# Performance work log

Hardware: AMD Instinct MI355X
Metric: run time of the kernel (lower is better)

## Reference

```python
import jax, jax.numpy as jnp
import numpy as np

N_NODES = 20000
DEG = 6
E = N_NODES * DEG  # 120000 edges == line-graph nodes
D_NODE, D_EDGE = 64, 16
HID, OUT = 128, 128
EPS = 1e-5


def setup_inputs() -> dict:
    key = jax.random.key(0)
    ks = jax.random.split(key, 8)
    rng = np.random.default_rng(0)
    # graph: each node is the source of DEG edges (direction='out' -> index_r = edge_index[0])
    src = np.repeat(np.arange(N_NODES), DEG)
    dst = rng.integers(0, N_NODES, E)
    edge_index = np.stack([src, dst]).astype(np.int64)
    # two_step_index: ordered pairs of distinct edges sharing a source node
    # (bipartite 2-hop, self loops removed), then GATConv add_self_loops re-appends (i,i)
    ii, jj = np.meshgrid(np.arange(DEG), np.arange(DEG), indexing='ij')
    off = ~np.eye(DEG, dtype=bool)
    ii, jj = ii[off], jj[off]  # DEG*(DEG-1) within-group pairs
    base = (np.arange(N_NODES) * DEG)[:, None]
    s2 = np.concatenate([(base + ii[None, :]).ravel(), np.arange(E)])
    d2 = np.concatenate([(base + jj[None, :]).ravel(), np.arange(E)])
    index_2step = np.stack([s2, d2]).astype(np.int64)  # [2, 720000]
    d_in = D_NODE + D_EDGE
    return {
        "edge_attr": jax.random.normal(ks[0], (E, D_EDGE), jnp.float32),
        "node_attr": jax.random.normal(ks[1], (N_NODES, D_NODE), jnp.float32),
        "bn0_g": jnp.ones((d_in,), jnp.float32),
        "bn0_b": jnp.zeros((d_in,), jnp.float32),
        "W1": jax.random.normal(ks[2], (d_in, HID), jnp.float32) / np.sqrt(d_in).astype(np.float32),
        "bn1_g": jnp.ones((HID,), jnp.float32),
        "bn1_b": jnp.zeros((HID,), jnp.float32),
        "Wg": jax.random.normal(ks[3], (HID, OUT), jnp.float32) / np.sqrt(HID).astype(np.float32),
        "att_src": jax.random.normal(ks[4], (OUT,), jnp.float32) * 0.1,
        "att_dst": jax.random.normal(ks[5], (OUT,), jnp.float32) * 0.1,
        "gat_bias": jnp.zeros((OUT,), jnp.float32),
        "bnf_g": jnp.ones((OUT,), jnp.float32),
        "bnf_b": jnp.zeros((OUT,), jnp.float32),
        "edge_index": jnp.asarray(edge_index),
        "index_2step": jnp.asarray(index_2step),
        "num_nodes": N_NODES,
    }


def batch_norm(x, g, b):
    # training-mode BatchNorm1d (biased variance), like the torch module default
    mu = x.mean(0)
    var = x.var(0)
    return (x - mu) * jax.lax.rsqrt(var + EPS) * g + b


def reference(edge_attr, node_attr, bn0_g, bn0_b, W1, bn1_g, bn1_b,
              Wg, att_src, att_dst, gat_bias, bnf_g, bnf_b,
              edge_index, index_2step, num_nodes):
    index_r = edge_index[0]  # [E] source node of each edge (direction='out')
    # h0: per-edge concat of source-node attrs and edge attrs  [E, Dn+De]
    h0 = jnp.concatenate([node_attr[index_r], edge_attr], axis=1)
    # linear encoder: BN -> Linear(no bias) -> BN -> ReLU (dropout p=0)
    h1 = jax.nn.relu(batch_norm(batch_norm(h0, bn0_g, bn0_b) @ W1, bn1_g, bn1_b))
    # --- GATConv (heads=1) on the line graph given by index_2step ---
    E_ = h1.shape[0]
    x = h1 @ Wg                 # [E, OUT]
    a_src = x @ att_src         # [E]
    a_dst = x @ att_dst         # [E]
    s, d = index_2step[0], index_2step[1]
    e = jax.nn.leaky_relu(a_src[s] + a_dst[d], 0.2)          # [E2]
    e = e - jax.ops.segment_max(e, d, num_segments=E_)[d]    # stable edge-softmax
    ex = jnp.exp(e)
    alpha = ex / (jax.ops.segment_sum(ex, d, num_segments=E_)[d] + 1e-16)
    h2 = jax.ops.segment_sum(alpha[:, None] * x[s], d, num_segments=E_) + gat_bias
    # --- global_add_pool keyed by source node id, then final BatchNorm ---
    h3 = jax.ops.segment_sum(h2, index_r, num_segments=num_nodes)  # [N, OUT]
    return batch_norm(h3, bnf_g, bnf_b)
```

## Files before the change

kernel.cpp:

```cpp
#include <hip/hip_runtime.h>

#define N_NODES 20000
#define DEG 6
#define E_EDGES 120000
#define EPS_BN 1e-5f

#define WS_S0SUM 0
#define WS_S0SQ  80
#define WS_S1SUM 160
#define WS_S1SQ  1184
#define WS_FSUM  2208
#define WS_FSQ   3232
#define WS_STATS_FLOATS 4256

#define LDA0 104
#define LDH1 136

typedef float f32x4 __attribute__((ext_vector_type(4)));
typedef short bf16x8 __attribute__((ext_vector_type(8)));

__device__ __forceinline__ unsigned short f2bf(float f) {
  unsigned u = __float_as_uint(f);
  u += 0x7fffu + ((u >> 16) & 1u);
  return (unsigned short)(u >> 16);
}
__device__ __forceinline__ unsigned pack2bf(float a, float b) {
  return (unsigned)f2bf(a) | ((unsigned)f2bf(b) << 16);
}
__device__ __forceinline__ bf16x8 load_w_frag(const float* __restrict__ W,
                                              int col, int k0, int kmax) {
  union { bf16x8 v; unsigned u[4]; } tmp;
  #pragma unroll
  for (int p = 0; p < 4; ++p) {
    int k = k0 + 2 * p;
    float a = (k < kmax) ? W[k * 128 + col] : 0.f;
    float b = (k + 1 < kmax) ? W[(k + 1) * 128 + col] : 0.f;
    tmp.u[p] = pack2bf(a, b);
  }
  return tmp.v;
}

__global__ __launch_bounds__(256) void k1_bn0_stats(
    const float* __restrict__ node_attr, const float* __restrict__ edge_attr,
    float* __restrict__ ws) {
  __shared__ float red[256];
  const int t = threadIdx.x;
  const int b = blockIdx.x;
  if (b < 128) {
    const int c = t & 63, rl = t >> 6;
    float s = 0.f, q = 0.f;
    for (int row = b * 4 + rl; row < N_NODES; row += 512) {
      float v = node_attr[row * 64 + c];
      s += v; q += v * v;
    }
    red[t] = s;
    __syncthreads();
    if (t < 64) atomicAdd(&ws[WS_S0SUM + t], red[t] + red[t + 64] + red[t + 128] + red[t + 192]);
    __syncthreads();
    red[t] = q;
    __syncthreads();
    if (t < 64) atomicAdd(&ws[WS_S0SQ + t], red[t] + red[t + 64] + red[t + 128] + red[t + 192]);
  } else {
    const int c = t & 15, rl = t >> 4;
    float s = 0.f, q = 0.f;
    for (int row = (b - 128) * 16 + rl; row < E_EDGES; row += 2048) {
      float v = edge_attr[row * 16 + c];
      s += v; q += v * v;
    }
    red[t] = s;
    __syncthreads();
    if (t < 16) {
      float tot = 0.f;
      #pragma unroll
      for (int k = 0; k < 16; ++k) tot += red[t + 16 * k];
      atomicAdd(&ws[WS_S0SUM + 64 + t], tot);
    }
    __syncthreads();
    red[t] = q;
    __syncthreads();
    if (t < 16) {
      float tot = 0.f;
      #pragma unroll
      for (int k = 0; k < 16; ++k) tot += red[t + 16 * k];
      atomicAdd(&ws[WS_S0SQ + 64 + t], tot);
    }
  }
}

__global__ __launch_bounds__(256, 4) void k2_bn1_stats(
    const float* __restrict__ node_attr, const float* __restrict__ edge_attr,
    const float* __restrict__ bn0_g, const float* __restrict__ bn0_b,
    const float* __restrict__ W1, float* __restrict__ ws) {
  __shared__ short h0s[48 * LDA0];
  __shared__ float sc0[80], sh0[80];
  const int t = threadIdx.x;
  if (t < 80) {
    float cnt = (t < 64) ? (float)N_NODES : (float)E_EDGES;
    float mu = ws[WS_S0SUM + t] / cnt;
    float var = ws[WS_S0SQ + t] / cnt - mu * mu;
    float sc = bn0_g[t] * rsqrtf(var + EPS_BN);
    sc0[t] = sc; sh0[t] = bn0_b[t] - mu * sc;
  }
  const int l = t & 63, wid = t >> 6;
  const int lm = l & 15, lq = l >> 4;
  const int Nb = wid * 32;
  bf16x8 w1f[2][3];
  #pragma unroll
  for (int nt = 0; nt < 2; ++nt)
    #pragma unroll
    for (int ks = 0; ks < 3; ++ks)
      w1f[nt][ks] = load_w_frag(W1, Nb + nt * 16 + lm, ks * 32 + lq * 8, 80);
  __syncthreads();
  const int ebase = blockIdx.x * 48;
  for (int i = t; i < 48 * 40; i += 256) {
    int row = i / 40, pc = i % 40, c = pc * 2;
    int ge = ebase + row;
    float a, b;
    if (c < 64) {
      const float* p = node_attr + (ge / DEG) * 64 + c;
      a = p[0]; b = p[1];
    } else {
      const float* p = edge_attr + ge * 16 + (c - 64);
      a = p[0]; b = p[1];
    }
    a = a * sc0[c] + sh0[c];
    b = b * sc0[c + 1] + sh0[c + 1];
    *(unsigned*)&h0s[row * LDA0 + c] = pack2bf(a, b);
  }
  for (int i = t; i < 48 * 8; i += 256) {
    int row = i >> 3, pc = i & 7;
    *(unsigned*)&h0s[row * LDA0 + 80 + pc * 2] = 0u;
  }
  __syncthreads();
  f32x4 acc[3][2] = {};
  #pragma unroll
  for (int ks = 0; ks < 3; ++ks) {
    bf16x8 a[3];
    #pragma unroll
    for (int mt = 0; mt < 3; ++mt)
      a[mt] = *(const bf16x8*)&h0s[(mt * 16 + lm) * LDA0 + ks * 32 + lq * 8];
    #pragma unroll
    for (int mt = 0; mt < 3; ++mt)
      #pragma unroll
      for (int nt = 0; nt < 2; ++nt)
        acc[mt][nt] = __builtin_amdgcn_mfma_f32_16x16x32_bf16(a[mt], w1f[nt][ks], acc[mt][nt], 0, 0, 0);
  }
  const int set = blockIdx.x & 7;
  #pragma unroll
  for (int nt = 0; nt < 2; ++nt) {
    float s = 0.f, q = 0.f;
    #pragma unroll
    for (int mt = 0; mt < 3; ++mt)
      #pragma unroll
      for (int r = 0; r < 4; ++r) {
        float v = acc[mt][nt][r];
        s += v; q += v * v;
      }
    s += __shfl_xor(s, 16); s += __shfl_xor(s, 32);
    q += __shfl_xor(q, 16); q += __shfl_xor(q, 32);
    if (l < 16) {
      int col = Nb + nt * 16 + lm;
      atomicAdd(&ws[WS_S1SUM + set * 128 + col], s);
      atomicAdd(&ws[WS_S1SQ + set * 128 + col], q);
    }
  }
}

__global__ __launch_bounds__(256, 4) void k3_fused(
    const float* __restrict__ node_attr, const float* __restrict__ edge_attr,
    const float* __restrict__ bn0_g, const float* __restrict__ bn0_b,
    const float* __restrict__ W1,
    const float* __restrict__ bn1_g, const float* __restrict__ bn1_b,
    const float* __restrict__ Wg,
    const float* __restrict__ att_src, const float* __restrict__ att_dst,
    const float* __restrict__ gat_bias,
    float* __restrict__ out, float* __restrict__ ws) {
  __shared__ short h0s[48 * LDA0];
  __shared__ short h1s[48 * LDH1];
  __shared__ float sc0[80], sh0[80];
  __shared__ float sc1[128], sh1[128];
  __shared__ float asP[4][48], adP[4][48];
  __shared__ float asS[48], adS[48], wS[48];
  __shared__ float alphaL[48][6];
  __shared__ float h3L[8 * 128];
  __shared__ float red[8][128];

  const int t = threadIdx.x;
  if (t < 80) {
    float cnt = (t < 64) ? (float)N_NODES : (float)E_EDGES;
    float mu = ws[WS_S0SUM + t] / cnt;
    float var = ws[WS_S0SQ + t] / cnt - mu * mu;
    float sc = bn0_g[t] * rsqrtf(var + EPS_BN);
    sc0[t] = sc; sh0[t] = bn0_b[t] - mu * sc;
  }
  if (t < 128) {
    float s = 0.f, q = 0.f;
    #pragma unroll
    for (int st = 0; st < 8; ++st) {
      s += ws[WS_S1SUM + st * 128 + t];
      q += ws[WS_S1SQ + st * 128 + t];
    }
    const float invE = 1.f / (float)E_EDGES;
    float mu = s * invE;
    float var = q * invE - mu * mu;
    float sc = bn1_g[t] * rsqrtf(var + EPS_BN);
    sc1[t] = sc; sh1[t] = bn1_b[t] - mu * sc;
  }
  *(f32x4*)&h3L[t * 4] = (f32x4){0.f, 0.f, 0.f, 0.f};

  const int l = t & 63, wid = t >> 6;
  const int lm = l & 15, lq = l >> 4;
  const int Nb = wid * 32;
  bf16x8 w1f[2][3], wgf[2][4];
  #pragma unroll
  for (int nt = 0; nt < 2; ++nt) {
    #pragma unroll
    for (int ks = 0; ks < 3; ++ks)
      w1f[nt][ks] = load_w_frag(W1, Nb + nt * 16 + lm, ks * 32 + lq * 8, 80);
    #pragma unroll
    for (int ks = 0; ks < 4; ++ks)
      wgf[nt][ks] = load_w_frag(Wg, Nb + nt * 16 + lm, ks * 32 + lq * 8, 128);
  }
  float atS[2], atD[2];
  #pragma unroll
  for (int nt = 0; nt < 2; ++nt) {
    int col = Nb + nt * 16 + lm;
    atS[nt] = att_src[col]; atD[nt] = att_dst[col];
  }
  __syncthreads();

  float scc[2], shc[2];
  #pragma unroll
  for (int nt = 0; nt < 2; ++nt) {
    int col = Nb + nt * 16 + lm;
    scc[nt] = sc1[col]; shc[nt] = sh1[col];
  }
  const int ebase = blockIdx.x * 48;
  for (int i = t; i < 48 * 40; i += 256) {
    int row = i / 40, pc = i % 40, c = pc * 2;
    int ge = ebase + row;
    float a, b;
    if (c < 64) {
      const float* p = node_attr + (ge / DEG) * 64 + c;
      a = p[0]; b = p[1];
    } else {
      const float* p = edge_attr + ge * 16 + (c - 64);
      a = p[0]; b = p[1];
    }
    a = a * sc0[c] + sh0[c];
    b = b * sc0[c + 1] + sh0[c + 1];
    *(unsigned*)&h0s[row * LDA0 + c] = pack2bf(a, b);
  }
  for (int i = t; i < 48 * 8; i += 256) {
    int row = i >> 3, pc = i & 7;
    *(unsigned*)&h0s[row * LDA0 + 80 + pc * 2] = 0u;
  }
  __syncthreads();
  {
    f32x4 acc1[3][2] = {};
    #pragma unroll
    for (int ks = 0; ks < 3; ++ks) {
      bf16x8 a[3];
      #pragma unroll
      for (int mt = 0; mt < 3; ++mt)
        a[mt] = *(const bf16x8*)&h0s[(mt * 16 + lm) * LDA0 + ks * 32 + lq * 8];
      #pragma unroll
      for (int mt = 0; mt < 3; ++mt)
        #pragma unroll
        for (int nt = 0; nt < 2; ++nt)
          acc1[mt][nt] = __builtin_amdgcn_mfma_f32_16x16x32_bf16(a[mt], w1f[nt][ks], acc1[mt][nt], 0, 0, 0);
    }
    #pragma unroll
    for (int mt = 0; mt < 3; ++mt)
      #pragma unroll
      for (int nt = 0; nt < 2; ++nt)
        #pragma unroll
        for (int r = 0; r < 4; ++r) {
          int row = mt * 16 + lq * 4 + r;
          int col = Nb + nt * 16 + lm;
          float v = fmaxf(acc1[mt][nt][r] * scc[nt] + shc[nt], 0.f);
          h1s[row * LDH1 + col] = (short)f2bf(v);
        }
  }
  __syncthreads();
  f32x4 acc2[3][2] = {};
  #pragma unroll
  for (int ks = 0; ks < 4; ++ks) {
    bf16x8 a[3];
    #pragma unroll
    for (int mt = 0; mt < 3; ++mt)
      a[mt] = *(const bf16x8*)&h1s[(mt * 16 + lm) * LDH1 + ks * 32 + lq * 8];
    #pragma unroll
    for (int mt = 0; mt < 3; ++mt)
      #pragma unroll
      for (int nt = 0; nt < 2; ++nt)
        acc2[mt][nt] = __builtin_amdgcn_mfma_f32_16x16x32_bf16(a[mt], wgf[nt][ks], acc2[mt][nt], 0, 0, 0);
  }
  {
    float ps[3][4], pd[3][4];
    #pragma unroll
    for (int mt = 0; mt < 3; ++mt)
      #pragma unroll
      for (int r = 0; r < 4; ++r) {
        ps[mt][r] = acc2[mt][0][r] * atS[0] + acc2[mt][1][r] * atS[1];
        pd[mt][r] = acc2[mt][0][r] * atD[0] + acc2[mt][1][r] * atD[1];
      }
    #pragma unroll
    for (int off = 1; off < 16; off <<= 1)
      #pragma unroll
      for (int mt = 0; mt < 3; ++mt)
        #pragma unroll
        for (int r = 0; r < 4; ++r) {
          ps[mt][r] += __shfl_xor(ps[mt][r], off);
          pd[mt][r] += __shfl_xor(pd[mt][r], off);
        }
    if (lm == 0) {
      #pragma unroll
      for (int mt = 0; mt < 3; ++mt)
        #pragma unroll
        for (int r = 0; r < 4; ++r) {
          int row = mt * 16 + lq * 4 + r;
          asP[wid][row] = ps[mt][r];
          adP[wid][row] = pd[mt][r];
        }
    }
  }
  __syncthreads();
  if (t < 48) {
    asS[t] = asP[0][t] + asP[1][t] + asP[2][t] + asP[3][t];
    adS[t] = adP[0][t] + adP[1][t] + adP[2][t] + adP[3][t];
  }
  __syncthreads();
  if (t < 48) {
    int n = t / 6, nb6 = n * 6;
    float ad = adS[t];
    float s6[6], m = -1e30f;
    #pragma unroll
    for (int i = 0; i < 6; ++i) {
      float s = asS[nb6 + i] + ad;
      s = (s > 0.f) ? s : 0.2f * s;
      s6[i] = s; m = fmaxf(m, s);
    }
    float ssum = 0.f, ex[6];
    #pragma unroll
    for (int i = 0; i < 6; ++i) { ex[i] = __expf(s6[i] - m); ssum += ex[i]; }
    float inv = 1.f / (ssum + 1e-16f);
    #pragma unroll
    for (int i = 0; i < 6; ++i) alphaL[t][i] = ex[i] * inv;
  }
  __syncthreads();
  if (t < 48) {
    int n = t / 6, i = t % 6;
    float w = 0.f;
    #pragma unroll
    for (int j = 0; j < 6; ++j) w += alphaL[n * 6 + j][i];
    wS[t] = w;
  }
  __syncthreads();
  #pragma unroll
  for (int mt = 0; mt < 3; ++mt)
    #pragma unroll
    for (int r = 0; r < 4; ++r) {
      int row = mt * 16 + lq * 4 + r;
      float w = wS[row];
      int nl = row / 6;
      #pragma unroll
      for (int nt = 0; nt < 2; ++nt)
        atomicAdd(&h3L[nl * 128 + Nb + nt * 16 + lm], w * acc2[mt][nt][r]);
    }
  __syncthreads();
  const int c4 = (t & 31) * 4, nslot = t >> 5;
  f32x4 v = *(f32x4*)&h3L[nslot * 128 + c4];
  const f32x4 gb = *(const f32x4*)&gat_bias[c4];
  v[0] += 6.f * gb[0]; v[1] += 6.f * gb[1];
  v[2] += 6.f * gb[2]; v[3] += 6.f * gb[3];
  *(f32x4*)&out[(blockIdx.x * 8 + nslot) * 128 + c4] = v;
  const int set = blockIdx.x & 7;
  #pragma unroll
  for (int j = 0; j < 4; ++j) red[nslot][c4 + j] = v[j];
  __syncthreads();
  if (t < 128) {
    float s = 0.f;
    #pragma unroll
    for (int k = 0; k < 8; ++k) s += red[k][t];
    atomicAdd(&ws[WS_FSUM + set * 128 + t], s);
  }
  __syncthreads();
  #pragma unroll
  for (int j = 0; j < 4; ++j) red[nslot][c4 + j] = v[j] * v[j];
  __syncthreads();
  if (t < 128) {
    float s = 0.f;
    #pragma unroll
    for (int k = 0; k < 8; ++k) s += red[k][t];
    atomicAdd(&ws[WS_FSQ + set * 128 + t], s);
  }
}

__global__ __launch_bounds__(256) void k4_final(
    float* __restrict__ out, const float* __restrict__ ws,
    const float* __restrict__ bnf_g, const float* __restrict__ bnf_b) {
  int idx4 = blockIdx.x * 256 + threadIdx.x;
  if (idx4 >= N_NODES * 128 / 4) return;
  int c0 = (idx4 & 31) << 2;
  float4 v = ((float4*)out)[idx4];
  float4 fsv = {0.f, 0.f, 0.f, 0.f}, fqv = {0.f, 0.f, 0.f, 0.f};
  #pragma unroll
  for (int s = 0; s < 8; ++s) {
    float4 a = *(const float4*)&ws[WS_FSUM + s * 128 + c0];
    float4 b = *(const float4*)&ws[WS_FSQ + s * 128 + c0];
    fsv.x += a.x; fsv.y += a.y; fsv.z += a.z; fsv.w += a.w;
    fqv.x += b.x; fqv.y += b.y; fqv.z += b.z; fqv.w += b.w;
  }
  float4 g4 = *(const float4*)&bnf_g[c0];
  float4 b4 = *(const float4*)&bnf_b[c0];
  const float invN = 1.f / (float)N_NODES;
  float mu, var, sc;
  mu = fsv.x * invN; var = fqv.x * invN - mu * mu; sc = g4.x * rsqrtf(var + EPS_BN);
  v.x = (v.x - mu) * sc + b4.x;
  mu = fsv.y * invN; var = fqv.y * invN - mu * mu; sc = g4.y * rsqrtf(var + EPS_BN);
  v.y = (v.y - mu) * sc + b4.y;
  mu = fsv.z * invN; var = fqv.z * invN - mu * mu; sc = g4.z * rsqrtf(var + EPS_BN);
  v.z = (v.z - mu) * sc + b4.z;
  mu = fsv.w * invN; var = fqv.w * invN - mu * mu; sc = g4.w * rsqrtf(var + EPS_BN);
  v.w = (v.w - mu) * sc + b4.w;
  ((float4*)out)[idx4] = v;
}

extern "C" void kernel_launch(void* const* d_in, const int* in_sizes, int n_in,
                              void* d_out, int out_size, void* d_ws, size_t ws_size,
                              hipStream_t stream) {
  const float* edge_attr = (const float*)d_in[0];
  const float* node_attr = (const float*)d_in[1];
  const float* bn0_g = (const float*)d_in[2];
  const float* bn0_b = (const float*)d_in[3];
  const float* W1    = (const float*)d_in[4];
  const float* bn1_g = (const float*)d_in[5];
  const float* bn1_b = (const float*)d_in[6];
  const float* Wg    = (const float*)d_in[7];
  const float* att_src = (const float*)d_in[8];
  const float* att_dst = (const float*)d_in[9];
  const float* gat_bias = (const float*)d_in[10];
  const float* bnf_g = (const float*)d_in[11];
  const float* bnf_b = (const float*)d_in[12];
  float* ws = (float*)d_ws;
  float* out = (float*)d_out;

  hipMemsetAsync(d_ws, 0, WS_STATS_FLOATS * sizeof(float), stream);
  k1_bn0_stats<<<256, 256, 0, stream>>>(node_attr, edge_attr, ws);
  k2_bn1_stats<<<E_EDGES / 48, 256, 0, stream>>>(node_attr, edge_attr, bn0_g, bn0_b, W1, ws);
  k3_fused<<<E_EDGES / 48, 256, 0, stream>>>(node_attr, edge_attr, bn0_g, bn0_b, W1,
                                             bn1_g, bn1_b, Wg, att_src, att_dst, gat_bias,
                                             out, ws);
  k4_final<<<2500, 256, 0, stream>>>(out, ws, bnf_g, bnf_b);
}
```

Baseline: 253.6 us.

## Pre-transpose weights to bf16 once and load MFMA fragments as vectors

Adds a prep kernel that converts W1 and Wg to bf16 in a column-major (transposed, K-padded) workspace layout. K2 and k3 then load each weight fragment with a single 16-byte vector load instead of eight strided fp32 loads plus conversion in every block. In k3, weight fragment loads move to just before each GEMM to shorten register live ranges, and launch bounds drop from 4 to 2 waves per SIMD. The cost is one extra kernel launch, and the lower occupancy hint may reduce latency hiding.

```diff
diff --git a/kernel.cpp b/kernel.cpp
--- a/kernel.cpp
+++ b/kernel.cpp
@@ -12,6 +12,8 @@
 #define WS_FSUM  2208
 #define WS_FSQ   3232
 #define WS_STATS_FLOATS 4256
+#define WS_WT1   4256
+#define WS_WGT   10400
 
 #define LDA0 104
 #define LDH1 136
@@ -27,17 +29,21 @@
 __device__ __forceinline__ unsigned pack2bf(float a, float b) {
   return (unsigned)f2bf(a) | ((unsigned)f2bf(b) << 16);
 }
-__device__ __forceinline__ bf16x8 load_w_frag(const float* __restrict__ W,
-                                              int col, int k0, int kmax) {
-  union { bf16x8 v; unsigned u[4]; } tmp;
-  #pragma unroll
-  for (int p = 0; p < 4; ++p) {
-    int k = k0 + 2 * p;
-    float a = (k < kmax) ? W[k * 128 + col] : 0.f;
-    float b = (k + 1 < kmax) ? W[(k + 1) * 128 + col] : 0.f;
-    tmp.u[p] = pack2bf(a, b);
-  }
-  return tmp.v;
+
+__global__ __launch_bounds__(256) void k0_prep(
+    const float* __restrict__ W1, const float* __restrict__ Wg,
+    float* __restrict__ ws) {
+  short* wt1 = (short*)(ws + WS_WT1);
+  short* wgt = (short*)(ws + WS_WGT);
+  const int t0 = blockIdx.x * 256 + threadIdx.x;
+  for (int i = t0; i < 128 * 96; i += 32 * 256) {
+    int col = i / 96, k = i % 96;
+    wt1[i] = (k < 80) ? (short)f2bf(W1[k * 128 + col]) : (short)0;
+  }
+  for (int i = t0; i < 128 * 128; i += 32 * 256) {
+    int col = i >> 7, k = i & 127;
+    wgt[i] = (short)f2bf(Wg[k * 128 + col]);
+  }
 }
 
 __global__ __launch_bounds__(256) void k1_bn0_stats(
@@ -87,10 +93,10 @@
   }
 }
 
-__global__ __launch_bounds__(256, 4) void k2_bn1_stats(
+__global__ __launch_bounds__(256, 2) void k2_bn1_stats(
     const float* __restrict__ node_attr, const float* __restrict__ edge_attr,
     const float* __restrict__ bn0_g, const float* __restrict__ bn0_b,
-    const float* __restrict__ W1, float* __restrict__ ws) {
+    float* __restrict__ ws) {
   __shared__ short h0s[48 * LDA0];
   __shared__ float sc0[80], sh0[80];
   const int t = threadIdx.x;
@@ -104,12 +110,13 @@
   const int l = t & 63, wid = t >> 6;
   const int lm = l & 15, lq = l >> 4;
   const int Nb = wid * 32;
+  const short* wt1 = (const short*)(ws + WS_WT1);
   bf16x8 w1f[2][3];
   #pragma unroll
   for (int nt = 0; nt < 2; ++nt)
     #pragma unroll
     for (int ks = 0; ks < 3; ++ks)
-      w1f[nt][ks] = load_w_frag(W1, Nb + nt * 16 + lm, ks * 32 + lq * 8, 80);
+      w1f[nt][ks] = *(const bf16x8*)&wt1[(Nb + nt * 16 + lm) * 96 + ks * 32 + lq * 8];
   __syncthreads();
   const int ebase = blockIdx.x * 48;
   for (int i = t; i < 48 * 40; i += 256) {
@@ -166,12 +173,10 @@
   }
 }
 
-__global__ __launch_bounds__(256, 4) void k3_fused(
+__global__ __launch_bounds__(256, 2) void k3_fused(
     const float* __restrict__ node_attr, const float* __restrict__ edge_attr,
     const float* __restrict__ bn0_g, const float* __restrict__ bn0_b,
-    const float* __restrict__ W1,
     const float* __restrict__ bn1_g, const float* __restrict__ bn1_b,
-    const float* __restrict__ Wg,
     const float* __restrict__ att_src, const float* __restrict__ att_dst,
     const float* __restrict__ gat_bias,
     float* __restrict__ out, float* __restrict__ ws) {
@@ -211,52 +216,44 @@
   const int l = t & 63, wid = t >> 6;
   const int lm = l & 15, lq = l >> 4;
   const int Nb = wid * 32;
-  bf16x8 w1f[2][3], wgf[2][4];
-  #pragma unroll
-  for (int nt = 0; nt < 2; ++nt) {
-    #pragma unroll
-    for (int ks = 0; ks < 3; ++ks)
-      w1f[nt][ks] = load_w_frag(W1, Nb + nt * 16 + lm, ks * 32 + lq * 8, 80);
-    #pragma unroll
-    for (int ks = 0; ks < 4; ++ks)
-      wgf[nt][ks] = load_w_frag(Wg, Nb + nt * 16 + lm, ks * 32 + lq * 8, 128);
-  }
-  float atS[2], atD[2];
-  #pragma unroll
-  for (int nt = 0; nt < 2; ++nt) {
-    int col = Nb + nt * 16 + lm;
-    atS[nt] = att_src[col]; atD[nt] = att_dst[col];
-  }
-  __syncthreads();
-
-  float scc[2], shc[2];
-  #pragma unroll
-  for (int nt = 0; nt < 2; ++nt) {
-    int col = Nb + nt * 16 + lm;
-    scc[nt] = sc1[col]; shc[nt] = sh1[col];
-  }
+  const short* wt1 = (const short*)(ws + WS_WT1);
+  const short* wgt = (const short*)(ws + WS_WGT);
   const int ebase = blockIdx.x * 48;
-  for (int i = t; i < 48 * 40; i += 256) {
-    int row = i / 40, pc = i % 40, c = pc * 2;
-    int ge = ebase + row;
-    float a, b;
-    if (c < 64) {
-      const float* p = node_attr + (ge / DEG) * 64 + c;
-      a = p[0]; b = p[1];
-    } else {
-      const float* p = edge_attr + ge * 16 + (c - 64);
-      a = p[0]; b = p[1];
-    }
-    a = a * sc0[c] + sh0[c];
-    b = b * sc0[c + 1] + sh0[c + 1];
-    *(unsigned*)&h0s[row * LDA0 + c] = pack2bf(a, b);
-  }
-  for (int i = t; i < 48 * 8; i += 256) {
-    int row = i >> 3, pc = i & 7;
-    *(unsigned*)&h0s[row * LDA0 + 80 + pc * 2] = 0u;
-  }
-  __syncthreads();
+  __syncthreads();
+
   {
+    bf16x8 w1f[2][3];
+    #pragma unroll
+    for (int nt = 0; nt < 2; ++nt)
+      #pragma unroll
+      for (int ks = 0; ks < 3; ++ks)
+        w1f[nt][ks] = *(const bf16x8*)&wt1[(Nb + nt * 16 + lm) * 96 + ks * 32 + lq * 8];
+    float scc[2], shc[2];
+    #pragma unroll
+    for (int nt = 0; nt < 2; ++nt) {
+      int col = Nb + nt * 16 + lm;
+      scc[nt] = sc1[col]; shc[nt] = sh1[col];
+    }
+    for (int i = t; i < 48 * 40; i += 256) {
+      int row = i / 40, pc = i % 40, c = pc * 2;
+      int ge = ebase + row;
+      float a, b;
+      if (c < 64) {
+        const float* p = node_attr + (ge / DEG) * 64 + c;
+        a = p[0]; b = p[1];
+      } else {
+        const float* p = edge_attr + ge * 16 + (c - 64);
+        a = p[0]; b = p[1];
+      }
+      a = a * sc0[c] + sh0[c];
+      b = b * sc0[c + 1] + sh0[c + 1];
+      *(unsigned*)&h0s[row * LDA0 + c] = pack2bf(a, b);
+    }
+    for (int i = t; i < 48 * 8; i += 256) {
+      int row = i >> 3, pc = i & 7;
+      *(unsigned*)&h0s[row * LDA0 + 80 + pc * 2] = 0u;
+    }
+    __syncthreads();
     f32x4 acc1[3][2] = {};
     #pragma unroll
     for (int ks = 0; ks < 3; ++ks) {
@@ -283,6 +280,19 @@
         }
   }
   __syncthreads();
+
+  bf16x8 wgf[2][4];
+  #pragma unroll
+  for (int nt = 0; nt < 2; ++nt)
+    #pragma unroll
+    for (int ks = 0; ks < 4; ++ks)
+      wgf[nt][ks] = *(const bf16x8*)&wgt[(Nb + nt * 16 + lm) * 128 + ks * 32 + lq * 8];
+  float atS[2], atD[2];
+  #pragma unroll
+  for (int nt = 0; nt < 2; ++nt) {
+    int col = Nb + nt * 16 + lm;
+    atS[nt] = att_src[col]; atD[nt] = att_dst[col];
+  }
   f32x4 acc2[3][2] = {};
   #pragma unroll
   for (int ks = 0; ks < 4; ++ks) {
@@ -447,10 +457,11 @@
   float* out = (float*)d_out;
 
   hipMemsetAsync(d_ws, 0, WS_STATS_FLOATS * sizeof(float), stream);
+  k0_prep<<<32, 256, 0, stream>>>(W1, Wg, ws);
   k1_bn0_stats<<<256, 256, 0, stream>>>(node_attr, edge_attr, ws);
-  k2_bn1_stats<<<E_EDGES / 48, 256, 0, stream>>>(node_attr, edge_attr, bn0_g, bn0_b, W1, ws);
-  k3_fused<<<E_EDGES / 48, 256, 0, stream>>>(node_attr, edge_attr, bn0_g, bn0_b, W1,
-                                             bn1_g, bn1_b, Wg, att_src, att_dst, gat_bias,
+  k2_bn1_stats<<<E_EDGES / 48, 256, 0, stream>>>(node_attr, edge_attr, bn0_g, bn0_b, ws);
+  k3_fused<<<E_EDGES / 48, 256, 0, stream>>>(node_attr, edge_attr, bn0_g, bn0_b,
+                                             bn1_g, bn1_b, att_src, att_dst, gat_bias,
                                              out, ws);
   k4_final<<<2500, 256, 0, stream>>>(out, ws, bnf_g, bnf_b);
 }
```

Result: no change. 250.0 us (-1.4%).
